# Optimization experiments

Hardware: AMD Instinct MI355X
Metric: run time of the kernel (lower is better)

Reference implementation:

```python
import jax, jax.numpy as jnp
import numpy as np

N = 50000       # nodes
E = 800000      # edges (avg degree 16)
D_IN = 128      # input_dim
HID = 128       # hidden_dim
G_FEAT = 32     # g_feat_dim
G = 64          # number of graphs in batch
EPS = 1e-5      # BatchNorm eps


def _lin_init(key, fan_in, fan_out):
    s = 1.0 / np.sqrt(fan_in)
    return jax.random.uniform(key, (fan_in, fan_out), jnp.float32, -s, s)


def setup_inputs() -> dict:
    key = jax.random.key(0)
    ks = jax.random.split(key, 24)
    inp = {
        'x': jax.random.normal(ks[0], (N, D_IN), jnp.float32),
        'edge_index': jax.random.randint(ks[1], (2, E), 0, N, jnp.int64),
        'batch': jnp.sort(jax.random.randint(ks[2], (N,), 0, G, jnp.int64)),
        'g_feats': jax.random.normal(ks[3], (G, G_FEAT), jnp.float32),
    }
    dims = [D_IN, HID, HID]
    k = 4
    for i, din in enumerate(dims):
        inp[f'Wl{i}'] = _lin_init(ks[k], din, HID); k += 1   # lin_l (neighbors, has bias)
        inp[f'bl{i}'] = jnp.zeros((HID,), jnp.float32)
        inp[f'Wr{i}'] = _lin_init(ks[k], din, HID); k += 1   # lin_r (self, no bias in PyG)
        inp[f'gamma{i}'] = jnp.ones((HID,), jnp.float32)
        inp[f'beta{i}'] = jnp.zeros((HID,), jnp.float32)
    inp['W1'] = _lin_init(ks[k], 2 * HID + G_FEAT, HID); k += 1
    inp['b1'] = jnp.zeros((HID,), jnp.float32)
    inp['W2'] = _lin_init(ks[k], HID, HID // 2); k += 1
    inp['b2'] = jnp.zeros((HID // 2,), jnp.float32)
    inp['W3'] = _lin_init(ks[k], HID // 2, 1); k += 1
    inp['b3'] = jnp.zeros((1,), jnp.float32)
    return inp


def _sage_conv(h, src, dst, Wl, bl, Wr):
    # mean-aggregate neighbor messages x_j into target i, then lin_l(agg)+lin_r(self)
    msgs = h[src]  # [E, d] irregular gather
    agg = jax.ops.segment_sum(msgs, dst, num_segments=N)
    cnt = jax.ops.segment_sum(jnp.ones((E,), h.dtype), dst, num_segments=N)
    agg = agg / jnp.clip(cnt, 1.0)[:, None]
    return agg @ Wl + bl + h @ Wr


def _batch_norm(h, gamma, beta):
    mu = jnp.mean(h, axis=0)
    var = jnp.var(h, axis=0)
    return gamma * (h - mu) * jax.lax.rsqrt(var + EPS) + beta


def _forward(x, edge_index, batch, g_feats, convs, head):
    src, dst = edge_index[0], edge_index[1]
    h = x
    for (Wl, bl, Wr, gamma, beta) in convs:
        h = jax.nn.relu(_batch_norm(_sage_conv(h, src, dst, Wl, bl, Wr), gamma, beta))
        # dropout p=0.01: identity in eval/reference mode
    cnt = jnp.clip(jax.ops.segment_sum(jnp.ones((N,), h.dtype), batch, num_segments=G), 1.0)
    hg_mean = jax.ops.segment_sum(h, batch, num_segments=G) / cnt[:, None]
    hg_max = jax.ops.segment_max(h, batch, num_segments=G)
    W1, b1, W2, b2, W3, b3 = head
    m = jnp.concatenate([hg_mean, hg_max, g_feats], axis=1)  # [G, 2*HID+G_FEAT]
    m = jax.nn.relu(m @ W1 + b1)
    m = jax.nn.relu(m @ W2 + b2)
    return (m @ W3 + b3).reshape(-1)  # [G]


def reference(x, edge_index, batch, g_feats,
              Wl0, bl0, Wr0, gamma0, beta0,
              Wl1, bl1, Wr1, gamma1, beta1,
              Wl2, bl2, Wr2, gamma2, beta2,
              W1, b1, W2, b2, W3, b3):
    convs = [(Wl0, bl0, Wr0, gamma0, beta0),
             (Wl1, bl1, Wr1, gamma1, beta1),
             (Wl2, bl2, Wr2, gamma2, beta2)]
    head = (W1, b1, W2, b2, W3, b3)
    return _forward(x, edge_index, batch, g_feats, convs, head)
```

## Files before the change

kernel.cpp:

```cpp
#include <hip/hip_runtime.h>
#include <stdint.h>

#define NN 50000
#define NE 800000
#define HID 128
#define NG 64
#define BN_EPS 1e-5f
#define SCAN_BLOCKS 196
#define GEMM_BLOCKS ((NN + 127) / 128)
#define SC_NB 8
#define SC_BSZ ((NN + SC_NB - 1) / SC_NB)
#define SC_CHUNK 4096
#define SC_CHUNKS ((NE + SC_CHUNK - 1) / SC_CHUNK)

typedef __bf16 bf16x8 __attribute__((ext_vector_type(8)));
typedef float floatx4 __attribute__((ext_vector_type(4)));

__device__ __forceinline__ float b2f(unsigned short u) {
    union { unsigned int i; float f; } x; x.i = ((unsigned int)u) << 16; return x.f;
}
__device__ __forceinline__ float blo(unsigned int d) { return __uint_as_float(d << 16); }
__device__ __forceinline__ float bhi(unsigned int d) { return __uint_as_float(d & 0xffff0000u); }
__device__ __forceinline__ unsigned short f2b(float f) {
    union { float f; unsigned int i; } x; x.f = f; unsigned int i = x.i;
    if ((i & 0x7f800000u) == 0x7f800000u) return (unsigned short)(i >> 16);
    return (unsigned short)((i + 0x7fffu + ((i >> 16) & 1u)) >> 16);
}
__device__ __forceinline__ unsigned int pack2(float f0, float f1) {
    return (((unsigned int)f2b(f1)) << 16) | f2b(f0);
}
__device__ __forceinline__ float2 bn_pair(const float* __restrict__ bnstat,
                                          const float* __restrict__ gamma,
                                          const float* __restrict__ beta, int c) {
    float mu = bnstat[c] * (1.f / NN);
    float var = bnstat[128 + c] * (1.f / NN) - mu * mu;
    float s = gamma[c] * rsqrtf(var + BN_EPS);
    return make_float2(s, beta[c] - mu * s);
}

__global__ void k_setup(const float* __restrict__ x, unsigned short* xb, int* deg,
                        int* gstart, int* gend, float* bnstats,
                        float* pool_sum, int* pool_max,
                        const float* __restrict__ Wl0, const float* __restrict__ Wr0,
                        const float* __restrict__ Wl1, const float* __restrict__ Wr1,
                        const float* __restrict__ Wl2, const float* __restrict__ Wr2,
                        unsigned short* Bp) {
    int i = blockIdx.x * 256 + threadIdx.x;
    if (i < NN * 64) {
        float2 v = ((const float2*)x)[i];
        ((unsigned int*)xb)[i] = pack2(v.x, v.y);
    }
    if (i < NN) deg[i] = 0;
    if (i < NG) { gstart[i] = NN; gend[i] = -1; }
    if (i < 3 * 256) bnstats[i] = 0.f;
    if (i < NG * HID) { pool_sum[i] = 0.f; pool_max[i] = 0; }
    if (i < 3 * 32768) {
        int layer = i >> 15;
        int r = i & 32767;
        int nt = r >> 12, kk = (r >> 9) & 7, l = (r >> 3) & 63, j = r & 7;
        int k = kk * 32 + (l >> 4) * 8 + j;
        int n = nt * 16 + (l & 15);
        const float* Wl = layer == 0 ? Wl0 : (layer == 1 ? Wl1 : Wl2);
        const float* Wr = layer == 0 ? Wr0 : (layer == 1 ? Wr1 : Wr2);
        Bp[i] = f2b((k < 128) ? Wl[k * 128 + n] : Wr[(k - 128) * 128 + n]);
    }
}

__global__ void k_hist(const int* __restrict__ dst, int* deg) {
    int bucket = blockIdx.x & (SC_NB - 1);
    int chunk = blockIdx.x / SC_NB;
    int lo = bucket * SC_BSZ, hi = lo + SC_BSZ;
    int base = chunk * SC_CHUNK;
#pragma unroll
    for (int i = 0; i < SC_CHUNK / 256; ++i) {
        int e = base + i * 256 + threadIdx.x;
        if (e < NE) {
            int d = dst[e];
            if (d >= lo && d < hi) atomicAdd(&deg[d], 1);
        }
    }
}

__global__ void k_scan1(const int* __restrict__ deg, int* blocksum,
                        const int* __restrict__ batch, int* gstart, int* gend) {
    __shared__ int lds[256];
    int t = threadIdx.x, i = blockIdx.x * 256 + t;
    lds[t] = (i < NN) ? deg[i] : 0;
    if (i < NN) {
        int g = batch[i];
        if (i == 0 || batch[i - 1] != g) atomicMin(&gstart[g], i);
        if (i == NN - 1 || batch[i + 1] != g) atomicMax(&gend[g], i);
    }
    __syncthreads();
    for (int off = 128; off > 0; off >>= 1) {
        if (t < off) lds[t] += lds[t + off];
        __syncthreads();
    }
    if (t == 0) blocksum[blockIdx.x] = lds[0];
}

__global__ void k_scan2(const int* __restrict__ blocksum, int* blockoff, int* row_start) {
    __shared__ int lds[256];
    int t = threadIdx.x;
    int v = (t < SCAN_BLOCKS) ? blocksum[t] : 0;
    lds[t] = v;
    __syncthreads();
    for (int off = 1; off < 256; off <<= 1) {
        int u = (t >= off) ? lds[t - off] : 0;
        __syncthreads();
        lds[t] += u;
        __syncthreads();
    }
    if (t < SCAN_BLOCKS) blockoff[t] = lds[t] - v;
    if (t == 255) row_start[NN] = lds[255];
}

__global__ void k_scan3(const int* __restrict__ deg, const int* __restrict__ blockoff,
                        int* row_start, int* cursor) {
    __shared__ int lds[256];
    int t = threadIdx.x, i = blockIdx.x * 256 + t;
    int v = (i < NN) ? deg[i] : 0;
    lds[t] = v;
    __syncthreads();
    for (int off = 1; off < 256; off <<= 1) {
        int u = (t >= off) ? lds[t - off] : 0;
        __syncthreads();
        lds[t] += u;
        __syncthreads();
    }
    if (i < NN) {
        int ex = blockoff[blockIdx.x] + lds[t] - v;
        row_start[i] = ex;
        cursor[i] = ex;
    }
}

__global__ void k_scatter(const int* __restrict__ src, const int* __restrict__ dst,
                          int* cursor, int* col) {
    int bucket = blockIdx.x & (SC_NB - 1);
    int chunk = blockIdx.x / SC_NB;
    int lo = bucket * SC_BSZ, hi = lo + SC_BSZ;
    int base = chunk * SC_CHUNK;
#pragma unroll
    for (int i = 0; i < SC_CHUNK / 256; ++i) {
        int e = base + i * 256 + threadIdx.x;
        if (e < NE) {
            int d = dst[e];
            if (d >= lo && d < hi) {
                int p = atomicAdd(&cursor[d], 1);
                col[p] = src[e];
            }
        }
    }
}

__global__ void k_agg(const unsigned short* __restrict__ h, const int* __restrict__ row_start,
                      const int* __restrict__ col, const float* __restrict__ bnstat,
                      const float* __restrict__ gamma, const float* __restrict__ beta,
                      unsigned short* __restrict__ agg) {
    int wid = threadIdx.x >> 6, lane = threadIdx.x & 63;
    int slot = lane >> 4, sub = lane & 15;
    int node = (blockIdx.x * 4 + wid) * 4 + slot;
    int s = row_start[node], e = row_start[node + 1];
    bool ap = bnstat != nullptr;
    float scv[8], shv[8];
    if (ap) {
#pragma unroll
        for (int i = 0; i < 8; ++i) {
            float2 p = bn_pair(bnstat, gamma, beta, sub * 8 + i);
            scv[i] = p.x; shv[i] = p.y;
        }
    }
    auto tf = [&](float f, int i) -> float {
        return ap ? fmaxf(f * scv[i] + shv[i], 0.f) : f;
    };
    const uint4* h4 = (const uint4*)h;
    float a0 = 0.f, a1 = 0.f, a2 = 0.f, a3 = 0.f, a4 = 0.f, a5 = 0.f, a6 = 0.f, a7 = 0.f;
    int j = s;
    for (; j + 4 <= e; j += 4) {
        int u0 = col[j], u1 = col[j + 1], u2 = col[j + 2], u3 = col[j + 3];
        uint4 v0 = h4[(size_t)u0 * 16 + sub];
        uint4 v1 = h4[(size_t)u1 * 16 + sub];
        uint4 v2 = h4[(size_t)u2 * 16 + sub];
        uint4 v3 = h4[(size_t)u3 * 16 + sub];
        a0 += (tf(blo(v0.x), 0) + tf(blo(v1.x), 0)) + (tf(blo(v2.x), 0) + tf(blo(v3.x), 0));
        a1 += (tf(bhi(v0.x), 1) + tf(bhi(v1.x), 1)) + (tf(bhi(v2.x), 1) + tf(bhi(v3.x), 1));
        a2 += (tf(blo(v0.y), 2) + tf(blo(v1.y), 2)) + (tf(blo(v2.y), 2) + tf(blo(v3.y), 2));
        a3 += (tf(bhi(v0.y), 3) + tf(bhi(v1.y), 3)) + (tf(bhi(v2.y), 3) + tf(bhi(v3.y), 3));
        a4 += (tf(blo(v0.z), 4) + tf(blo(v1.z), 4)) + (tf(blo(v2.z), 4) + tf(blo(v3.z), 4));
        a5 += (tf(bhi(v0.z), 5) + tf(bhi(v1.z), 5)) + (tf(bhi(v2.z), 5) + tf(bhi(v3.z), 5));
        a6 += (tf(blo(v0.w), 6) + tf(blo(v1.w), 6)) + (tf(blo(v2.w), 6) + tf(blo(v3.w), 6));
        a7 += (tf(bhi(v0.w), 7) + tf(bhi(v1.w), 7)) + (tf(bhi(v2.w), 7) + tf(bhi(v3.w), 7));
    }
    for (; j < e; ++j) {
        int u = col[j];
        uint4 v = h4[(size_t)u * 16 + sub];
        a0 += tf(blo(v.x), 0);  a1 += tf(bhi(v.x), 1);
        a2 += tf(blo(v.y), 2);  a3 += tf(bhi(v.y), 3);
        a4 += tf(blo(v.z), 4);  a5 += tf(bhi(v.z), 5);
        a6 += tf(blo(v.w), 6);  a7 += tf(bhi(v.w), 7);
    }
    float inv = (e > s) ? 1.f / (float)(e - s) : 0.f;
    uint4 o;
    o.x = pack2(a0 * inv, a1 * inv);
    o.y = pack2(a2 * inv, a3 * inv);
    o.z = pack2(a4 * inv, a5 * inv);
    o.w = pack2(a6 * inv, a7 * inv);
    ((uint4*)agg)[(size_t)node * 16 + sub] = o;
}

__device__ __forceinline__ bf16x8 norm8(bf16x8 v, const float* sc, const float* sh, int cbase) {
    union { bf16x8 v; unsigned short u[8]; } in; in.v = v;
    union { unsigned int u[4]; bf16x8 v; } out;
#pragma unroll
    for (int i = 0; i < 4; ++i) {
        float f0 = fmaxf(b2f(in.u[2 * i]) * sc[cbase + 2 * i] + sh[cbase + 2 * i], 0.f);
        float f1 = fmaxf(b2f(in.u[2 * i + 1]) * sc[cbase + 2 * i + 1] + sh[cbase + 2 * i + 1], 0.f);
        out.u[i] = pack2(f0, f1);
    }
    return out.v;
}

__global__ void __launch_bounds__(256) k_gemm(unsigned short* buf,
                                              const unsigned short* h,
                                              const unsigned short* __restrict__ Bp,
                                              const float* __restrict__ pbnstat,
                                              const float* __restrict__ pgamma,
                                              const float* __restrict__ pbeta,
                                              float* bnstat) {
    __shared__ unsigned short Bs[32768];
    __shared__ float s_sc[128], s_sh[128];
    int t = threadIdx.x;
    {
        const uint4* s4 = (const uint4*)Bp;
        uint4* d4 = (uint4*)Bs;
        for (int i = t; i < 4096; i += 256) d4[i] = s4[i];
    }
    bool ap = pbnstat != nullptr;
    if (ap && t < 128) {
        float2 p = bn_pair(pbnstat, pgamma, pbeta, t);
        s_sc[t] = p.x; s_sh[t] = p.y;
    }
    __syncthreads();
    int wid = t >> 6, lane = t & 63;
    int m = lane & 15, q = lane >> 4;
    int mbase = blockIdx.x * 128 + wid * 32;
    bool active = mbase < NN;
    float s8[8] = {0, 0, 0, 0, 0, 0, 0, 0};
    float ss8[8] = {0, 0, 0, 0, 0, 0, 0, 0};
    if (active) {
        int row0 = mbase + m;
        int row1 = min(mbase + 16 + m, NN - 1);
        const bf16x8* Abuf = (const bf16x8*)buf;
        const bf16x8* Ah = (const bf16x8*)h;
        size_t b0 = (size_t)row0 * 16, b1 = (size_t)row1 * 16;
        bf16x8 af0[8], af1[8];
#pragma unroll
        for (int kk = 0; kk < 4; ++kk) {
            af0[kk] = Abuf[b0 + kk * 4 + q];
            af1[kk] = Abuf[b1 + kk * 4 + q];
            bf16x8 h0 = Ah[b0 + kk * 4 + q];
            bf16x8 h1 = Ah[b1 + kk * 4 + q];
            if (ap) {
                int cb = kk * 32 + q * 8;
                h0 = norm8(h0, s_sc, s_sh, cb);
                h1 = norm8(h1, s_sc, s_sh, cb);
            }
            af0[4 + kk] = h0;
            af1[4 + kk] = h1;
        }
        const bf16x8* B = (const bf16x8*)Bs;
        floatx4 acc[2][8];
#pragma unroll
        for (int mt = 0; mt < 2; ++mt)
#pragma unroll
            for (int nt = 0; nt < 8; ++nt) acc[mt][nt] = (floatx4){0.f, 0.f, 0.f, 0.f};
#pragma unroll
        for (int kk = 0; kk < 8; ++kk) {
#pragma unroll
            for (int nt = 0; nt < 8; ++nt) {
                bf16x8 b = B[(nt * 8 + kk) * 64 + lane];
                acc[0][nt] = __builtin_amdgcn_mfma_f32_16x16x32_bf16(af0[kk], b, acc[0][nt], 0, 0, 0);
                acc[1][nt] = __builtin_amdgcn_mfma_f32_16x16x32_bf16(af1[kk], b, acc[1][nt], 0, 0, 0);
            }
        }
#pragma unroll
        for (int mt = 0; mt < 2; ++mt)
#pragma unroll
            for (int nt = 0; nt < 8; ++nt) {
                int c = nt * 16 + m;
#pragma unroll
                for (int reg = 0; reg < 4; ++reg) {
                    int r = mbase + mt * 16 + q * 4 + reg;
                    if (r < NN) {
                        float v = acc[mt][nt][reg];
                        buf[(size_t)r * 128 + c] = f2b(v);
                        s8[nt] += v;
                        ss8[nt] += v * v;
                    }
                }
            }
#pragma unroll
        for (int nt = 0; nt < 8; ++nt) {
            s8[nt] += __shfl_xor(s8[nt], 16, 64);  s8[nt] += __shfl_xor(s8[nt], 32, 64);
            ss8[nt] += __shfl_xor(ss8[nt], 16, 64); ss8[nt] += __shfl_xor(ss8[nt], 32, 64);
        }
    }
    __syncthreads();
    float* stf = (float*)Bs;
    if (t < 256) stf[t] = 0.f;
    __syncthreads();
    if (active && lane < 16) {
#pragma unroll
        for (int nt = 0; nt < 8; ++nt) {
            int c = nt * 16 + m;
            atomicAdd(&stf[c], s8[nt]);
            atomicAdd(&stf[128 + c], ss8[nt]);
        }
    }
    __syncthreads();
    if (t < 256) atomicAdd(&bnstat[t], stf[t]);
}

__global__ void k_pool(const unsigned short* __restrict__ h, const int* __restrict__ gstart,
                       const int* __restrict__ gend, const float* __restrict__ bnstat,
                       const float* __restrict__ gamma, const float* __restrict__ beta,
                       float* pool_sum, int* pool_max) {
    int g = blockIdx.x >> 3, chunk = blockIdx.x & 7;
    int s = gstart[g], e = gend[g];
    if (s > e) return;
    int cnt = e - s + 1;
    int per = (cnt + 7) >> 3;
    int r0 = s + chunk * per;
    int r1 = min(r0 + per, e + 1);
    int c = threadIdx.x & 127, half = threadIdx.x >> 7;
    float2 pr = bn_pair(bnstat, gamma, beta, c);
    float sm = 0.f, mx = 0.f;
    for (int r = r0 + half; r < r1; r += 2) {
        float v = fmaxf(b2f(h[(size_t)r * 128 + c]) * pr.x + pr.y, 0.f);
        sm += v;
        mx = fmaxf(mx, v);
    }
    atomicAdd(&pool_sum[g * 128 + c], sm);
    atomicMax(&pool_max[g * 128 + c], __float_as_int(mx));
}

__global__ void __launch_bounds__(128) k_head(
    const float* __restrict__ pool_sum, const int* __restrict__ pool_max,
    const int* __restrict__ gstart, const int* __restrict__ gend,
    const float* __restrict__ gfeats,
    const float* __restrict__ W1, const float* __restrict__ bs1,
    const float* __restrict__ W2, const float* __restrict__ bs2,
    const float* __restrict__ W3, const float* __restrict__ bs3,
    float* out) {
    __shared__ float m[288];
    __shared__ float o1[128];
    __shared__ float o2[64];
    int g = blockIdx.x, t = threadIdx.x;
    int s = gstart[g], e = gend[g];
    int cint = e - s + 1;
    float cnt = (float)(cint < 1 ? 1 : cint);
    if (t < 128) {
        m[t] = pool_sum[g * 128 + t] / cnt;
        m[128 + t] = __int_as_float(pool_max[g * 128 + t]);
    }
    if (t < 32) m[256 + t] = gfeats[g * 32 + t];
    __syncthreads();
    float acc = bs1[t];
    for (int k = 0; k < 288; ++k) acc += m[k] * W1[k * 128 + t];
    o1[t] = fmaxf(acc, 0.f);
    __syncthreads();
    if (t < 64) {
        float a2 = bs2[t];
        for (int k = 0; k < 128; ++k) a2 += o1[k] * W2[k * 64 + t];
        o2[t] = fmaxf(a2, 0.f);
    }
    __syncthreads();
    if (t < 64) {
        float p = o2[t] * W3[t];
#pragma unroll
        for (int off = 32; off; off >>= 1) p += __shfl_down(p, off, 64);
        if (t == 0) out[g] = p + bs3[0];
    }
}

extern "C" void kernel_launch(void* const* d_in, const int* in_sizes, int n_in,
                              void* d_out, int out_size, void* d_ws, size_t ws_size,
                              hipStream_t stream) {
    const float* x = (const float*)d_in[0];
    const int* ei = (const int*)d_in[1];
    const int* batch = (const int*)d_in[2];
    const float* gfeats = (const float*)d_in[3];
    const float *Wl[3], *Wr[3], *gma[3], *bta[3];
    for (int i = 0; i < 3; ++i) {
        Wl[i] = (const float*)d_in[4 + 5 * i];
        Wr[i] = (const float*)d_in[6 + 5 * i];
        gma[i] = (const float*)d_in[7 + 5 * i];
        bta[i] = (const float*)d_in[8 + 5 * i];
    }
    const float* W1 = (const float*)d_in[19];
    const float* bs1 = (const float*)d_in[20];
    const float* W2 = (const float*)d_in[21];
    const float* bs2 = (const float*)d_in[22];
    const float* W3 = (const float*)d_in[23];
    const float* bs3 = (const float*)d_in[24];

    char* p = (char*)d_ws;
    auto alloc = [&](size_t bytes) -> char* {
        char* r = p;
        p += (bytes + 255) & ~(size_t)255;
        return r;
    };
    int* deg = (int*)alloc(NN * 4);
    int* row_start = (int*)alloc((NN + 1) * 4);
    int* cursor = (int*)alloc(NN * 4);
    int* col = (int*)alloc(NE * 4);
    int* gstart = (int*)alloc(NG * 4);
    int* gend = (int*)alloc(NG * 4);
    float* bnstats = (float*)alloc(3 * 256 * 4);
    float* pool_sum = (float*)alloc(NG * HID * 4);
    int* pool_max = (int*)alloc(NG * HID * 4);
    int* blocksum = (int*)alloc(SCAN_BLOCKS * 4);
    int* blockoff = (int*)alloc(SCAN_BLOCKS * 4);
    unsigned short* Bp = (unsigned short*)alloc(3 * 32768 * 2);
    unsigned short* xb = (unsigned short*)alloc((size_t)NN * 128 * 2);
    unsigned short* b0 = (unsigned short*)alloc((size_t)NN * 128 * 2);
    unsigned short* b1 = (unsigned short*)alloc((size_t)NN * 128 * 2);

    const int* srcv = ei;
    const int* dstv = ei + NE;

    k_setup<<<(NN * 64 + 255) / 256, 256, 0, stream>>>(
        x, xb, deg, gstart, gend, bnstats, pool_sum, pool_max,
        Wl[0], Wr[0], Wl[1], Wr[1], Wl[2], Wr[2], Bp);
    k_hist<<<SC_CHUNKS * SC_NB, 256, 0, stream>>>(dstv, deg);
    k_scan1<<<SCAN_BLOCKS, 256, 0, stream>>>(deg, blocksum, batch, gstart, gend);
    k_scan2<<<1, 256, 0, stream>>>(blocksum, blockoff, row_start);
    k_scan3<<<SCAN_BLOCKS, 256, 0, stream>>>(deg, blockoff, row_start, cursor);
    k_scatter<<<SC_CHUNKS * SC_NB, 256, 0, stream>>>(srcv, dstv, cursor, col);

    const unsigned short* hin = xb;
    unsigned short* work[3] = {b0, b1, b0};
    for (int l = 0; l < 3; ++l) {
        unsigned short* w = work[l];
        const float* pb = (l == 0) ? nullptr : bnstats + (l - 1) * 256;
        const float* pg = (l == 0) ? nullptr : gma[l - 1];
        const float* pt = (l == 0) ? nullptr : bta[l - 1];
        k_agg<<<(NN + 15) / 16, 256, 0, stream>>>(hin, row_start, col, pb, pg, pt, w);
        k_gemm<<<GEMM_BLOCKS, 256, 0, stream>>>(w, hin, Bp + l * 32768, pb, pg, pt,
                                                bnstats + l * 256);
        hin = w;
    }
    k_pool<<<NG * 8, 256, 0, stream>>>(hin, gstart, gend, bnstats + 2 * 256, gma[2], bta[2],
                                       pool_sum, pool_max);
    k_head<<<NG, 128, 0, stream>>>(pool_sum, pool_max, gstart, gend, gfeats,
                                   W1, bs1, W2, bs2, W3, bs3, (float*)d_out);
}
```

Baseline: 402.3 us.

## Store node features in 32-column slices and aggregate one slice per launch

Node feature buffers now use a sliced layout: four planes, each holding 32 bf16 columns for every node. The aggregation runs four times per layer, once per slice, with 4 lanes per node, so each gather pass touches a working set a quarter the size, which may fit in L2/MALL. The setup, GEMM, and pooling indexing is updated to match. In exchange, row_start and col are re-read four times and there are more launches, and each gather is a 64-byte segment per node.

```diff
diff --git a/kernel.cpp b/kernel.cpp
--- a/kernel.cpp
+++ b/kernel.cpp
@@ -13,6 +13,7 @@
 #define SC_CHUNK 4096
 #define SC_CHUNKS ((NE + SC_CHUNK - 1) / SC_CHUNK)
 
+
 typedef __bf16 bf16x8 __attribute__((ext_vector_type(8)));
 typedef float floatx4 __attribute__((ext_vector_type(4)));
 
@@ -47,8 +48,10 @@
                         unsigned short* Bp) {
     int i = blockIdx.x * 256 + threadIdx.x;
     if (i < NN * 64) {
+        int row = i >> 6, cp = i & 63;
         float2 v = ((const float2*)x)[i];
-        ((unsigned int*)xb)[i] = pack2(v.x, v.y);
+        size_t o = (size_t)(cp >> 4) * NN * 16 + (size_t)row * 16 + (cp & 15);
+        ((unsigned int*)xb)[o] = pack2(v.x, v.y);
     }
     if (i < NN) deg[i] = 0;
     if (i < NG) { gstart[i] = NN; gend[i] = -1; }
@@ -157,32 +160,34 @@
 __global__ void k_agg(const unsigned short* __restrict__ h, const int* __restrict__ row_start,
                       const int* __restrict__ col, const float* __restrict__ bnstat,
                       const float* __restrict__ gamma, const float* __restrict__ beta,
-                      unsigned short* __restrict__ agg) {
+                      unsigned short* __restrict__ agg, int slice) {
     int wid = threadIdx.x >> 6, lane = threadIdx.x & 63;
-    int slot = lane >> 4, sub = lane & 15;
-    int node = (blockIdx.x * 4 + wid) * 4 + slot;
+    int nw = lane >> 2, sub = lane & 3;
+    int node = blockIdx.x * 64 + wid * 16 + nw;
+    if (node >= NN) return;
     int s = row_start[node], e = row_start[node + 1];
     bool ap = bnstat != nullptr;
     float scv[8], shv[8];
+    int cbase = slice * 32 + sub * 8;
     if (ap) {
 #pragma unroll
         for (int i = 0; i < 8; ++i) {
-            float2 p = bn_pair(bnstat, gamma, beta, sub * 8 + i);
+            float2 p = bn_pair(bnstat, gamma, beta, cbase + i);
             scv[i] = p.x; shv[i] = p.y;
         }
     }
     auto tf = [&](float f, int i) -> float {
         return ap ? fmaxf(f * scv[i] + shv[i], 0.f) : f;
     };
-    const uint4* h4 = (const uint4*)h;
+    const uint4* h4 = (const uint4*)h + (size_t)slice * NN * 4;
     float a0 = 0.f, a1 = 0.f, a2 = 0.f, a3 = 0.f, a4 = 0.f, a5 = 0.f, a6 = 0.f, a7 = 0.f;
     int j = s;
     for (; j + 4 <= e; j += 4) {
         int u0 = col[j], u1 = col[j + 1], u2 = col[j + 2], u3 = col[j + 3];
-        uint4 v0 = h4[(size_t)u0 * 16 + sub];
-        uint4 v1 = h4[(size_t)u1 * 16 + sub];
-        uint4 v2 = h4[(size_t)u2 * 16 + sub];
-        uint4 v3 = h4[(size_t)u3 * 16 + sub];
+        uint4 v0 = h4[(size_t)u0 * 4 + sub];
+        uint4 v1 = h4[(size_t)u1 * 4 + sub];
+        uint4 v2 = h4[(size_t)u2 * 4 + sub];
+        uint4 v3 = h4[(size_t)u3 * 4 + sub];
         a0 += (tf(blo(v0.x), 0) + tf(blo(v1.x), 0)) + (tf(blo(v2.x), 0) + tf(blo(v3.x), 0));
         a1 += (tf(bhi(v0.x), 1) + tf(bhi(v1.x), 1)) + (tf(bhi(v2.x), 1) + tf(bhi(v3.x), 1));
         a2 += (tf(blo(v0.y), 2) + tf(blo(v1.y), 2)) + (tf(blo(v2.y), 2) + tf(blo(v3.y), 2));
@@ -194,7 +199,7 @@
     }
     for (; j < e; ++j) {
         int u = col[j];
-        uint4 v = h4[(size_t)u * 16 + sub];
+        uint4 v = h4[(size_t)u * 4 + sub];
         a0 += tf(blo(v.x), 0);  a1 += tf(bhi(v.x), 1);
         a2 += tf(blo(v.y), 2);  a3 += tf(bhi(v.y), 3);
         a4 += tf(blo(v.z), 4);  a5 += tf(bhi(v.z), 5);
@@ -206,7 +211,7 @@
     o.y = pack2(a2 * inv, a3 * inv);
     o.z = pack2(a4 * inv, a5 * inv);
     o.w = pack2(a6 * inv, a7 * inv);
-    ((uint4*)agg)[(size_t)node * 16 + sub] = o;
+    ((uint4*)agg)[(size_t)slice * NN * 4 + (size_t)node * 4 + sub] = o;
 }
 
 __device__ __forceinline__ bf16x8 norm8(bf16x8 v, const float* sc, const float* sh, int cbase) {
@@ -253,14 +258,15 @@
         int row1 = min(mbase + 16 + m, NN - 1);
         const bf16x8* Abuf = (const bf16x8*)buf;
         const bf16x8* Ah = (const bf16x8*)h;
-        size_t b0 = (size_t)row0 * 16, b1 = (size_t)row1 * 16;
         bf16x8 af0[8], af1[8];
 #pragma unroll
         for (int kk = 0; kk < 4; ++kk) {
-            af0[kk] = Abuf[b0 + kk * 4 + q];
-            af1[kk] = Abuf[b1 + kk * 4 + q];
-            bf16x8 h0 = Ah[b0 + kk * 4 + q];
-            bf16x8 h1 = Ah[b1 + kk * 4 + q];
+            size_t base0 = ((size_t)kk * NN + row0) * 4 + q;
+            size_t base1 = ((size_t)kk * NN + row1) * 4 + q;
+            af0[kk] = Abuf[base0];
+            af1[kk] = Abuf[base1];
+            bf16x8 h0 = Ah[base0];
+            bf16x8 h1 = Ah[base1];
             if (ap) {
                 int cb = kk * 32 + q * 8;
                 h0 = norm8(h0, s_sc, s_sh, cb);
@@ -289,12 +295,13 @@
 #pragma unroll
             for (int nt = 0; nt < 8; ++nt) {
                 int c = nt * 16 + m;
+                int sl = c >> 5, cw = c & 31;
 #pragma unroll
                 for (int reg = 0; reg < 4; ++reg) {
                     int r = mbase + mt * 16 + q * 4 + reg;
                     if (r < NN) {
                         float v = acc[mt][nt][reg];
-                        buf[(size_t)r * 128 + c] = f2b(v);
+                        buf[((size_t)sl * NN + r) * 32 + cw] = f2b(v);
                         s8[nt] += v;
                         ss8[nt] += v * v;
                     }
@@ -335,9 +342,10 @@
     int r1 = min(r0 + per, e + 1);
     int c = threadIdx.x & 127, half = threadIdx.x >> 7;
     float2 pr = bn_pair(bnstat, gamma, beta, c);
+    size_t sbase = (size_t)(c >> 5) * NN * 32 + (c & 31);
     float sm = 0.f, mx = 0.f;
     for (int r = r0 + half; r < r1; r += 2) {
-        float v = fmaxf(b2f(h[(size_t)r * 128 + c]) * pr.x + pr.y, 0.f);
+        float v = fmaxf(b2f(h[sbase + (size_t)r * 32]) * pr.x + pr.y, 0.f);
         sm += v;
         mx = fmaxf(mx, v);
     }
@@ -446,7 +454,8 @@
         const float* pb = (l == 0) ? nullptr : bnstats + (l - 1) * 256;
         const float* pg = (l == 0) ? nullptr : gma[l - 1];
         const float* pt = (l == 0) ? nullptr : bta[l - 1];
-        k_agg<<<(NN + 15) / 16, 256, 0, stream>>>(hin, row_start, col, pb, pg, pt, w);
+        for (int s = 0; s < 4; ++s)
+            k_agg<<<(NN + 63) / 64, 256, 0, stream>>>(hin, row_start, col, pb, pg, pt, w, s);
         k_gemm<<<GEMM_BLOCKS, 256, 0, stream>>>(w, hin, Bp + l * 32768, pb, pg, pt,
                                                 bnstats + l * 256);
         hin = w;
```

New measurement: 475.5 us. +18.2%, slower.

## Fuse neighbor aggregation into layer GEMM, merge scans, fold pooling into head

Applied to the files above, without the earlier changes.

The separate aggregation kernel is removed. Each layer kernel now gathers and mean-aggregates neighbor rows (with the previous layer's BatchNorm+ReLU applied) directly into its MFMA A-fragments, so the aggregated buffer is never written to or read from global memory. The three-kernel degree scan becomes one 1024-thread block that also records graph start and end. The pooling kernel and its atomics are folded into the head kernel, which pools each graph in-block. The trade-off is that the irregular gather now runs at the GEMM kernel's much lower block count and occupancy (64KB LDS per block), which may expose gather latency.

```diff
diff --git a/kernel.cpp b/kernel.cpp
--- a/kernel.cpp
+++ b/kernel.cpp
@@ -6,12 +6,12 @@
 #define HID 128
 #define NG 64
 #define BN_EPS 1e-5f
-#define SCAN_BLOCKS 196
 #define GEMM_BLOCKS ((NN + 127) / 128)
 #define SC_NB 8
 #define SC_BSZ ((NN + SC_NB - 1) / SC_NB)
 #define SC_CHUNK 4096
 #define SC_CHUNKS ((NE + SC_CHUNK - 1) / SC_CHUNK)
+#define SCAN_TILES 49
 
 typedef __bf16 bf16x8 __attribute__((ext_vector_type(8)));
 typedef float floatx4 __attribute__((ext_vector_type(4)));
@@ -40,7 +40,6 @@
 
 __global__ void k_setup(const float* __restrict__ x, unsigned short* xb, int* deg,
                         int* gstart, int* gend, float* bnstats,
-                        float* pool_sum, int* pool_max,
                         const float* __restrict__ Wl0, const float* __restrict__ Wr0,
                         const float* __restrict__ Wl1, const float* __restrict__ Wr1,
                         const float* __restrict__ Wl2, const float* __restrict__ Wr2,
@@ -53,7 +52,6 @@
     if (i < NN) deg[i] = 0;
     if (i < NG) { gstart[i] = NN; gend[i] = -1; }
     if (i < 3 * 256) bnstats[i] = 0.f;
-    if (i < NG * HID) { pool_sum[i] = 0.f; pool_max[i] = 0; }
     if (i < 3 * 32768) {
         int layer = i >> 15;
         int r = i & 32767;
@@ -81,58 +79,53 @@
     }
 }
 
-__global__ void k_scan1(const int* __restrict__ deg, int* blocksum,
-                        const int* __restrict__ batch, int* gstart, int* gend) {
-    __shared__ int lds[256];
-    int t = threadIdx.x, i = blockIdx.x * 256 + t;
-    lds[t] = (i < NN) ? deg[i] : 0;
-    if (i < NN) {
-        int g = batch[i];
-        if (i == 0 || batch[i - 1] != g) atomicMin(&gstart[g], i);
-        if (i == NN - 1 || batch[i + 1] != g) atomicMax(&gend[g], i);
-    }
-    __syncthreads();
-    for (int off = 128; off > 0; off >>= 1) {
-        if (t < off) lds[t] += lds[t + off];
+__global__ void __launch_bounds__(1024) k_scan(const int* __restrict__ deg,
+                                               const int* __restrict__ batch,
+                                               int* row_start, int* cursor,
+                                               int* gstart, int* gend) {
+    __shared__ int ws[1024];
+    int t = threadIdx.x, lane = t & 63, w = t >> 6;
+    for (int j = 0; j < SCAN_TILES; ++j) {
+        int idx = j * 1024 + t;
+        int v = (idx < NN) ? deg[idx] : 0;
+#pragma unroll
+        for (int off = 32; off; off >>= 1) v += __shfl_xor(v, off, 64);
+        if (lane == 0) ws[j * 16 + w] = v;
+    }
+    __syncthreads();
+    int sv = (t < SCAN_TILES * 16) ? ws[t] : 0;
+    __syncthreads();
+    ws[t] = sv;
+    __syncthreads();
+    for (int off = 1; off < 1024; off <<= 1) {
+        int u = (t >= off) ? ws[t - off] : 0;
         __syncthreads();
-    }
-    if (t == 0) blocksum[blockIdx.x] = lds[0];
-}
-
-__global__ void k_scan2(const int* __restrict__ blocksum, int* blockoff, int* row_start) {
-    __shared__ int lds[256];
-    int t = threadIdx.x;
-    int v = (t < SCAN_BLOCKS) ? blocksum[t] : 0;
-    lds[t] = v;
-    __syncthreads();
-    for (int off = 1; off < 256; off <<= 1) {
-        int u = (t >= off) ? lds[t - off] : 0;
+        ws[t] += u;
         __syncthreads();
-        lds[t] += u;
-        __syncthreads();
-    }
-    if (t < SCAN_BLOCKS) blockoff[t] = lds[t] - v;
-    if (t == 255) row_start[NN] = lds[255];
-}
-
-__global__ void k_scan3(const int* __restrict__ deg, const int* __restrict__ blockoff,
-                        int* row_start, int* cursor) {
-    __shared__ int lds[256];
-    int t = threadIdx.x, i = blockIdx.x * 256 + t;
-    int v = (i < NN) ? deg[i] : 0;
-    lds[t] = v;
-    __syncthreads();
-    for (int off = 1; off < 256; off <<= 1) {
-        int u = (t >= off) ? lds[t - off] : 0;
-        __syncthreads();
-        lds[t] += u;
-        __syncthreads();
-    }
-    if (i < NN) {
-        int ex = blockoff[blockIdx.x] + lds[t] - v;
-        row_start[i] = ex;
-        cursor[i] = ex;
-    }
+    }
+    int inc = ws[t];
+    __syncthreads();
+    ws[t] = inc - sv;
+    __syncthreads();
+    for (int j = 0; j < SCAN_TILES; ++j) {
+        int idx = j * 1024 + t;
+        int v = (idx < NN) ? deg[idx] : 0;
+        int sc = v;
+#pragma unroll
+        for (int off = 1; off < 64; off <<= 1) {
+            int u = __shfl_up(sc, off, 64);
+            if (lane >= off) sc += u;
+        }
+        if (idx < NN) {
+            int ex = ws[j * 16 + w] + sc - v;
+            row_start[idx] = ex;
+            cursor[idx] = ex;
+            int g = batch[idx];
+            if (idx == 0 || batch[idx - 1] != g) gstart[g] = idx;
+            if (idx == NN - 1 || batch[idx + 1] != g) gend[g] = idx;
+        }
+    }
+    if (t == 0) row_start[NN] = NE;
 }
 
 __global__ void k_scatter(const int* __restrict__ src, const int* __restrict__ dst,
@@ -154,35 +147,22 @@
     }
 }
 
-__global__ void k_agg(const unsigned short* __restrict__ h, const int* __restrict__ row_start,
-                      const int* __restrict__ col, const float* __restrict__ bnstat,
-                      const float* __restrict__ gamma, const float* __restrict__ beta,
-                      unsigned short* __restrict__ agg) {
-    int wid = threadIdx.x >> 6, lane = threadIdx.x & 63;
-    int slot = lane >> 4, sub = lane & 15;
-    int node = (blockIdx.x * 4 + wid) * 4 + slot;
-    int s = row_start[node], e = row_start[node + 1];
-    bool ap = bnstat != nullptr;
-    float scv[8], shv[8];
-    if (ap) {
-#pragma unroll
-        for (int i = 0; i < 8; ++i) {
-            float2 p = bn_pair(bnstat, gamma, beta, sub * 8 + i);
-            scv[i] = p.x; shv[i] = p.y;
-        }
-    }
+template <int AP>
+__device__ __forceinline__ void gather_row(const uint4* __restrict__ h4,
+                                           const int* __restrict__ col, int s, int e,
+                                           int ci, const float* sc8, const float* sh8,
+                                           bf16x8* out) {
+    float a0 = 0.f, a1 = 0.f, a2 = 0.f, a3 = 0.f, a4 = 0.f, a5 = 0.f, a6 = 0.f, a7 = 0.f;
     auto tf = [&](float f, int i) -> float {
-        return ap ? fmaxf(f * scv[i] + shv[i], 0.f) : f;
+        return AP ? fmaxf(f * sc8[i] + sh8[i], 0.f) : f;
     };
-    const uint4* h4 = (const uint4*)h;
-    float a0 = 0.f, a1 = 0.f, a2 = 0.f, a3 = 0.f, a4 = 0.f, a5 = 0.f, a6 = 0.f, a7 = 0.f;
     int j = s;
     for (; j + 4 <= e; j += 4) {
         int u0 = col[j], u1 = col[j + 1], u2 = col[j + 2], u3 = col[j + 3];
-        uint4 v0 = h4[(size_t)u0 * 16 + sub];
-        uint4 v1 = h4[(size_t)u1 * 16 + sub];
-        uint4 v2 = h4[(size_t)u2 * 16 + sub];
-        uint4 v3 = h4[(size_t)u3 * 16 + sub];
+        uint4 v0 = h4[(size_t)u0 * 16 + ci];
+        uint4 v1 = h4[(size_t)u1 * 16 + ci];
+        uint4 v2 = h4[(size_t)u2 * 16 + ci];
+        uint4 v3 = h4[(size_t)u3 * 16 + ci];
         a0 += (tf(blo(v0.x), 0) + tf(blo(v1.x), 0)) + (tf(blo(v2.x), 0) + tf(blo(v3.x), 0));
         a1 += (tf(bhi(v0.x), 1) + tf(bhi(v1.x), 1)) + (tf(bhi(v2.x), 1) + tf(bhi(v3.x), 1));
         a2 += (tf(blo(v0.y), 2) + tf(blo(v1.y), 2)) + (tf(blo(v2.y), 2) + tf(blo(v3.y), 2));
@@ -194,19 +174,19 @@
     }
     for (; j < e; ++j) {
         int u = col[j];
-        uint4 v = h4[(size_t)u * 16 + sub];
+        uint4 v = h4[(size_t)u * 16 + ci];
         a0 += tf(blo(v.x), 0);  a1 += tf(bhi(v.x), 1);
         a2 += tf(blo(v.y), 2);  a3 += tf(bhi(v.y), 3);
         a4 += tf(blo(v.z), 4);  a5 += tf(bhi(v.z), 5);
         a6 += tf(blo(v.w), 6);  a7 += tf(bhi(v.w), 7);
     }
     float inv = (e > s) ? 1.f / (float)(e - s) : 0.f;
-    uint4 o;
-    o.x = pack2(a0 * inv, a1 * inv);
-    o.y = pack2(a2 * inv, a3 * inv);
-    o.z = pack2(a4 * inv, a5 * inv);
-    o.w = pack2(a6 * inv, a7 * inv);
-    ((uint4*)agg)[(size_t)node * 16 + sub] = o;
+    union { uint4 u; bf16x8 v; } o;
+    o.u.x = pack2(a0 * inv, a1 * inv);
+    o.u.y = pack2(a2 * inv, a3 * inv);
+    o.u.z = pack2(a4 * inv, a5 * inv);
+    o.u.w = pack2(a6 * inv, a7 * inv);
+    *out = o.v;
 }
 
 __device__ __forceinline__ bf16x8 norm8(bf16x8 v, const float* sc, const float* sh, int cbase) {
@@ -221,13 +201,16 @@
     return out.v;
 }
 
-__global__ void __launch_bounds__(256) k_gemm(unsigned short* buf,
-                                              const unsigned short* h,
-                                              const unsigned short* __restrict__ Bp,
-                                              const float* __restrict__ pbnstat,
-                                              const float* __restrict__ pgamma,
-                                              const float* __restrict__ pbeta,
-                                              float* bnstat) {
+template <int AP>
+__global__ void __launch_bounds__(256) k_layer(const unsigned short* __restrict__ h,
+                                               const int* __restrict__ row_start,
+                                               const int* __restrict__ col,
+                                               const unsigned short* __restrict__ Bp,
+                                               const float* __restrict__ pbnstat,
+                                               const float* __restrict__ pgamma,
+                                               const float* __restrict__ pbeta,
+                                               float* bnstat,
+                                               unsigned short* __restrict__ out) {
     __shared__ unsigned short Bs[32768];
     __shared__ float s_sc[128], s_sh[128];
     int t = threadIdx.x;
@@ -236,8 +219,7 @@
         uint4* d4 = (uint4*)Bs;
         for (int i = t; i < 4096; i += 256) d4[i] = s4[i];
     }
-    bool ap = pbnstat != nullptr;
-    if (ap && t < 128) {
+    if (AP && t < 128) {
         float2 p = bn_pair(pbnstat, pgamma, pbeta, t);
         s_sc[t] = p.x; s_sh[t] = p.y;
     }
@@ -249,19 +231,34 @@
     float s8[8] = {0, 0, 0, 0, 0, 0, 0, 0};
     float ss8[8] = {0, 0, 0, 0, 0, 0, 0, 0};
     if (active) {
-        int row0 = mbase + m;
-        int row1 = min(mbase + 16 + m, NN - 1);
-        const bf16x8* Abuf = (const bf16x8*)buf;
+        int r0 = mbase + m, r1 = mbase + 16 + m;
+        const uint4* h4 = (const uint4*)h;
+        int s0 = 0, e0 = 0, s1 = 0, e1 = 0;
+        if (r0 < NN) { s0 = row_start[r0]; e0 = row_start[r0 + 1]; }
+        if (r1 < NN) { s1 = row_start[r1]; e1 = row_start[r1 + 1]; }
+        bf16x8 af0[8], af1[8];
+#pragma unroll
+        for (int kk = 0; kk < 4; ++kk) {
+            float sc8[8], sh8[8];
+            if (AP) {
+#pragma unroll
+                for (int i = 0; i < 8; ++i) {
+                    sc8[i] = s_sc[kk * 32 + q * 8 + i];
+                    sh8[i] = s_sh[kk * 32 + q * 8 + i];
+                }
+            }
+            int ci = kk * 4 + q;
+            gather_row<AP>(h4, col, s0, e0, ci, sc8, sh8, &af0[kk]);
+            gather_row<AP>(h4, col, s1, e1, ci, sc8, sh8, &af1[kk]);
+        }
+        int r0c = min(r0, NN - 1), r1c = min(r1, NN - 1);
         const bf16x8* Ah = (const bf16x8*)h;
-        size_t b0 = (size_t)row0 * 16, b1 = (size_t)row1 * 16;
-        bf16x8 af0[8], af1[8];
+        size_t hb0 = (size_t)r0c * 16, hb1 = (size_t)r1c * 16;
 #pragma unroll
         for (int kk = 0; kk < 4; ++kk) {
-            af0[kk] = Abuf[b0 + kk * 4 + q];
-            af1[kk] = Abuf[b1 + kk * 4 + q];
-            bf16x8 h0 = Ah[b0 + kk * 4 + q];
-            bf16x8 h1 = Ah[b1 + kk * 4 + q];
-            if (ap) {
+            bf16x8 h0 = Ah[hb0 + kk * 4 + q];
+            bf16x8 h1 = Ah[hb1 + kk * 4 + q];
+            if (AP) {
                 int cb = kk * 32 + q * 8;
                 h0 = norm8(h0, s_sc, s_sh, cb);
                 h1 = norm8(h1, s_sc, s_sh, cb);
@@ -294,7 +291,7 @@
                     int r = mbase + mt * 16 + q * 4 + reg;
                     if (r < NN) {
                         float v = acc[mt][nt][reg];
-                        buf[(size_t)r * 128 + c] = f2b(v);
+                        out[(size_t)r * 128 + c] = f2b(v);
                         s8[nt] += v;
                         ss8[nt] += v * v;
                     }
@@ -322,33 +319,11 @@
     if (t < 256) atomicAdd(&bnstat[t], stf[t]);
 }
 
-__global__ void k_pool(const unsigned short* __restrict__ h, const int* __restrict__ gstart,
-                       const int* __restrict__ gend, const float* __restrict__ bnstat,
-                       const float* __restrict__ gamma, const float* __restrict__ beta,
-                       float* pool_sum, int* pool_max) {
-    int g = blockIdx.x >> 3, chunk = blockIdx.x & 7;
-    int s = gstart[g], e = gend[g];
-    if (s > e) return;
-    int cnt = e - s + 1;
-    int per = (cnt + 7) >> 3;
-    int r0 = s + chunk * per;
-    int r1 = min(r0 + per, e + 1);
-    int c = threadIdx.x & 127, half = threadIdx.x >> 7;
-    float2 pr = bn_pair(bnstat, gamma, beta, c);
-    float sm = 0.f, mx = 0.f;
-    for (int r = r0 + half; r < r1; r += 2) {
-        float v = fmaxf(b2f(h[(size_t)r * 128 + c]) * pr.x + pr.y, 0.f);
-        sm += v;
-        mx = fmaxf(mx, v);
-    }
-    atomicAdd(&pool_sum[g * 128 + c], sm);
-    atomicMax(&pool_max[g * 128 + c], __float_as_int(mx));
-}
-
-__global__ void __launch_bounds__(128) k_head(
-    const float* __restrict__ pool_sum, const int* __restrict__ pool_max,
+__global__ void __launch_bounds__(512) k_head(
+    const unsigned short* __restrict__ h,
     const int* __restrict__ gstart, const int* __restrict__ gend,
-    const float* __restrict__ gfeats,
+    const float* __restrict__ bnstat, const float* __restrict__ gamma,
+    const float* __restrict__ beta, const float* __restrict__ gfeats,
     const float* __restrict__ W1, const float* __restrict__ bs1,
     const float* __restrict__ W2, const float* __restrict__ bs2,
     const float* __restrict__ W3, const float* __restrict__ bs3,
@@ -356,19 +331,33 @@
     __shared__ float m[288];
     __shared__ float o1[128];
     __shared__ float o2[64];
+    __shared__ float psum[512];
+    __shared__ float pmax[512];
     int g = blockIdx.x, t = threadIdx.x;
     int s = gstart[g], e = gend[g];
+    int c = t & 127, part = t >> 7;
+    float2 pr = bn_pair(bnstat, gamma, beta, c);
+    float sm = 0.f, mx = 0.f;
+    for (int r = s + part; r <= e; r += 4) {
+        float v = fmaxf(b2f(h[(size_t)r * 128 + c]) * pr.x + pr.y, 0.f);
+        sm += v;
+        mx = fmaxf(mx, v);
+    }
+    psum[t] = sm; pmax[t] = mx;
+    __syncthreads();
     int cint = e - s + 1;
     float cnt = (float)(cint < 1 ? 1 : cint);
     if (t < 128) {
-        m[t] = pool_sum[g * 128 + t] / cnt;
-        m[128 + t] = __int_as_float(pool_max[g * 128 + t]);
-    }
-    if (t < 32) m[256 + t] = gfeats[g * 32 + t];
-    __syncthreads();
-    float acc = bs1[t];
-    for (int k = 0; k < 288; ++k) acc += m[k] * W1[k * 128 + t];
-    o1[t] = fmaxf(acc, 0.f);
+        m[t] = (psum[t] + psum[t + 128] + psum[t + 256] + psum[t + 384]) / cnt;
+        m[128 + t] = fmaxf(fmaxf(pmax[t], pmax[t + 128]), fmaxf(pmax[t + 256], pmax[t + 384]));
+    }
+    if (t >= 128 && t < 160) m[256 + t - 128] = gfeats[g * 32 + t - 128];
+    __syncthreads();
+    if (t < 128) {
+        float acc = bs1[t];
+        for (int k = 0; k < 288; ++k) acc += m[k] * W1[k * 128 + t];
+        o1[t] = fmaxf(acc, 0.f);
+    }
     __syncthreads();
     if (t < 64) {
         float a2 = bs2[t];
@@ -418,10 +407,6 @@
     int* gstart = (int*)alloc(NG * 4);
     int* gend = (int*)alloc(NG * 4);
     float* bnstats = (float*)alloc(3 * 256 * 4);
-    float* pool_sum = (float*)alloc(NG * HID * 4);
-    int* pool_max = (int*)alloc(NG * HID * 4);
-    int* blocksum = (int*)alloc(SCAN_BLOCKS * 4);
-    int* blockoff = (int*)alloc(SCAN_BLOCKS * 4);
     unsigned short* Bp = (unsigned short*)alloc(3 * 32768 * 2);
     unsigned short* xb = (unsigned short*)alloc((size_t)NN * 128 * 2);
     unsigned short* b0 = (unsigned short*)alloc((size_t)NN * 128 * 2);
@@ -431,28 +416,27 @@
     const int* dstv = ei + NE;
 
     k_setup<<<(NN * 64 + 255) / 256, 256, 0, stream>>>(
-        x, xb, deg, gstart, gend, bnstats, pool_sum, pool_max,
+        x, xb, deg, gstart, gend, bnstats,
         Wl[0], Wr[0], Wl[1], Wr[1], Wl[2], Wr[2], Bp);
     k_hist<<<SC_CHUNKS * SC_NB, 256, 0, stream>>>(dstv, deg);
-    k_scan1<<<SCAN_BLOCKS, 256, 0, stream>>>(deg, blocksum, batch, gstart, gend);
-    k_scan2<<<1, 256, 0, stream>>>(blocksum, blockoff, row_start);
-    k_scan3<<<SCAN_BLOCKS, 256, 0, stream>>>(deg, blockoff, row_start, cursor);
+    k_scan<<<1, 1024, 0, stream>>>(deg, batch, row_start, cursor, gstart, gend);
     k_scatter<<<SC_CHUNKS * SC_NB, 256, 0, stream>>>(srcv, dstv, cursor, col);
 
     const unsigned short* hin = xb;
     unsigned short* work[3] = {b0, b1, b0};
     for (int l = 0; l < 3; ++l) {
         unsigned short* w = work[l];
-        const float* pb = (l == 0) ? nullptr : bnstats + (l - 1) * 256;
-        const float* pg = (l == 0) ? nullptr : gma[l - 1];
-        const float* pt = (l == 0) ? nullptr : bta[l - 1];
-        k_agg<<<(NN + 15) / 16, 256, 0, stream>>>(hin, row_start, col, pb, pg, pt, w);
-        k_gemm<<<GEMM_BLOCKS, 256, 0, stream>>>(w, hin, Bp + l * 32768, pb, pg, pt,
-                                                bnstats + l * 256);
+        if (l == 0) {
+            k_layer<0><<<GEMM_BLOCKS, 256, 0, stream>>>(hin, row_start, col, Bp,
+                                                        nullptr, nullptr, nullptr,
+                                                        bnstats, w);
+        } else {
+            k_layer<1><<<GEMM_BLOCKS, 256, 0, stream>>>(hin, row_start, col, Bp + l * 32768,
+                                                        bnstats + (l - 1) * 256, gma[l - 1],
+                                                        bta[l - 1], bnstats + l * 256, w);
+        }
         hin = w;
     }
-    k_pool<<<NG * 8, 256, 0, stream>>>(hin, gstart, gend, bnstats + 2 * 256, gma[2], bta[2],
-                                       pool_sum, pool_max);
-    k_head<<<NG, 128, 0, stream>>>(pool_sum, pool_max, gstart, gend, gfeats,
-                                   W1, bs1, W2, bs2, W3, bs3, (float*)d_out);
-}
+    k_head<<<NG, 512, 0, stream>>>(hin, gstart, gend, bnstats + 2 * 256, gma[2], bta[2],
+                                   gfeats, W1, bs1, W2, bs2, W3, bs3, (float*)d_out);
+}
```

After: 590.1 us. 46.7% more time.
